# Optimization experiments

Measured on AMD Instinct MI355X. Metric: run time of the kernel, lower is better.

## Reference

```python
import jax, jax.numpy as jnp
import numpy as np

B, C_IN, T = 16, 1, 10240
C = 256                # conv_dim_out == config.model.conv_channels
KERNEL, STRIDE, PAD = 10, 5, 0
K_STEPS = 12           # config.model.predict_steps
NEG = 10               # config.train.neg_samples
EPS = 1e-5
L_OUT = (T + 2 * PAD - KERNEL) // STRIDE + 1   # 2047


def setup_inputs() -> dict:
    key = jax.random.key(0)
    ks = jax.random.split(key, 5)
    return {
        "x": jax.random.normal(ks[0], (B, C_IN, T), jnp.float32),
        "conv_w": jax.random.normal(ks[1], (C, C_IN, KERNEL), jnp.float32) * 0.1,
        "conv_b": jnp.zeros((C,), jnp.float32),
        "bn_gamma": jnp.ones((C,), jnp.float32),
        "bn_beta": jnp.zeros((C,), jnp.float32),
        "tr_w": jax.random.normal(ks[2], (K_STEPS, C, C), jnp.float32) / np.sqrt(C).astype(np.float32),
        "tr_b": jnp.zeros((K_STEPS, C), jnp.float32),
        "perm": jax.random.permutation(ks[3], L_OUT),  # randperm over the time axis
    }


def reference(x, conv_w, conv_b, bn_gamma, bn_beta, tr_w, tr_b, perm):
    # ---- encoder: Conv1d -> ReLU -> BatchNorm1d (training-mode batch stats) ----
    h = jax.lax.conv_general_dilated(
        x, conv_w, window_strides=(STRIDE,), padding=[(PAD, PAD)],
        dimension_numbers=("NCH", "OIH", "NCH"))
    h = jax.nn.relu(h + conv_b[None, :, None])            # (B, C, L)
    mu = h.mean(axis=(0, 2), keepdims=True)
    var = h.var(axis=(0, 2), keepdims=True)               # biased, as torch BN
    h = (h - mu) * jax.lax.rsqrt(var + EPS)
    h = h * bn_gamma[None, :, None] + bn_beta[None, :, None]
    z = h.transpose(0, 2, 1)                              # (B, L, C)

    # ---- negatives: batch-roll by 1, random permutation of the time axis; detached ----
    z_negative = jax.lax.stop_gradient(jnp.roll(z, 1, axis=0)[:, perm, :])

    L = z.shape[1]
    # z_neg_full[b, i] == roll(z_neg, i, axis=0)[b] == z_neg[(b - i) % B]
    roll_idx = (jnp.arange(B)[:, None] - jnp.arange(NEG)[None, :]) % B  # (B, NEG)

    losses = []
    for k in range(1, K_STEPS + 1):
        l_len = L - k
        z_pos = z[:, k:, :]                               # (B, l, C)
        z_neg = z_negative[:, k:, :]                      # (B, l, C)
        z_neg_full = z_neg[roll_idx]                      # (B, NEG, l, C)
        W, bb = tr_w[k - 1], tr_b[k - 1]
        est_pos = (z_pos @ W + bb)[:, None]               # (B, 1, l, C)
        est_neg = z_neg_full @ W + bb                     # (B, NEG, l, C)
        estimated = jnp.concatenate([est_pos, est_neg], axis=1)        # (B, S, l, C)
        z_full = jnp.concatenate([z_pos[:, None], z_neg_full], axis=1)  # (B, S, l, C)
        f = jnp.einsum("bslc,bslc->bsl", estimated, z_full)
        # faithful to torch: flatten (b, s, l) row-major then view as (b*l, S)
        f_k = f.reshape(B * l_len, NEG + 1)
        logp = jax.nn.log_softmax(f_k, axis=1)
        losses.append(-logp.sum() / ((l_len - k) * B))

    # torch forward returns z.permute(0, 2, 1); losses returned too for baseline use
    return z.transpose(0, 2, 1), jnp.stack(losses)
```

## Files before the change

kernel.cpp:

```cpp
#include <hip/hip_runtime.h>
#include <hip/hip_bf16.h>
#include <math.h>

constexpr int B_ = 16;
constexpr int T_ = 10240;
constexpr int C_ = 256;
constexpr int KW = 10;
constexpr int L_ = 2047;
constexpr int N_ = B_ * L_;
constexpr int KSTEPS = 12;
constexpr float EPS_ = 1e-5f;
constexpr int QSTR = 32768;

typedef short bf16x8 __attribute__((ext_vector_type(8)));
typedef float f32x4  __attribute__((ext_vector_type(4)));

__global__ __launch_bounds__(256) void stats_wt_kernel(
    const float* __restrict__ x, const float* __restrict__ cw, const float* __restrict__ cb,
    float* __restrict__ ssum, float* __restrict__ ssq,
    const float* __restrict__ tw, __hip_bfloat16* __restrict__ Wt)
{
    __shared__ float smem[64 * 65];
    const int bid = blockIdx.x;
    if (bid < 512) {
        const int b  = bid & 15;
        const int l0 = (bid >> 4) * 64;
        const int cnt = min(64, L_ - l0);
        const int c = threadIdx.x;
        float* xs = smem;
        const float* xb = x + (size_t)b * T_;
        for (int i = threadIdx.x; i < cnt * 5 + 5; i += 256) xs[i] = xb[l0 * 5 + i];
        float w[KW];
#pragma unroll
        for (int j = 0; j < KW; ++j) w[j] = cw[c * KW + j];
        const float bias = cb[c];
        __syncthreads();
        float s = 0.f, s2 = 0.f;
        float xw[KW];
#pragma unroll
        for (int j = 0; j < KW; ++j) xw[j] = xs[j];
#pragma unroll 2
        for (int dl = 0; dl < cnt; ++dl) {
            float v = bias;
#pragma unroll
            for (int j = 0; j < KW; ++j) v = fmaf(xw[j], w[j], v);
            v = fmaxf(v, 0.f);
            s += v;
            s2 = fmaf(v, v, s2);
#pragma unroll
            for (int j = 0; j < 5; ++j) xw[j] = xw[j + 5];
#pragma unroll
            for (int j = 0; j < 5; ++j) xw[j + 5] = xs[dl * 5 + 10 + j];
        }
        atomicAdd(&ssum[c], s);
        atomicAdd(&ssq[c], s2);
    } else {
        const int idx = bid - 512;
        const int k  = idx >> 4;
        const int c0 = ((idx & 15) >> 2) * 64, j0 = (idx & 3) * 64;
        float (*tile)[65] = (float(*)[65])smem;
        for (int i = threadIdx.x; i < 64 * 64; i += 256) {
            int c = i >> 6, j = i & 63;
            tile[c][j] = tw[((size_t)k * C_ + (c0 + c)) * C_ + j0 + j];
        }
        __syncthreads();
        for (int i = threadIdx.x; i < 64 * 64; i += 256) {
            int j = i >> 6, c = i & 63;
            Wt[((size_t)k * C_ + (j0 + j)) * C_ + c0 + c] = __float2bfloat16(tile[c][j]);
        }
    }
}

__global__ __launch_bounds__(256) void conv_norm_kernel(
    const float* __restrict__ x, const float* __restrict__ cw, const float* __restrict__ cb,
    const float* __restrict__ ssum, const float* __restrict__ ssq,
    const float* __restrict__ gamma, const float* __restrict__ beta,
    __hip_bfloat16* __restrict__ Zb, float* __restrict__ out0)
{
    const int b  = blockIdx.y;
    const int l0 = blockIdx.x * 32;
    const int cnt = min(32, L_ - l0);
    const int c = threadIdx.x;
    __shared__ float xs[32 * 5 + 8];
    __shared__ float zt[32][257];
    const float* xb = x + (size_t)b * T_;
    for (int i = threadIdx.x; i < cnt * 5 + 5; i += 256) xs[i] = xb[l0 * 5 + i];
    float w[KW];
#pragma unroll
    for (int j = 0; j < KW; ++j) w[j] = cw[c * KW + j];
    const float bias = cb[c];
    const float inv_n = 1.0f / (float)N_;
    const float mu  = ssum[c] * inv_n;
    const float var = ssq[c] * inv_n - mu * mu;
    const float sc  = gamma[c] * rsqrtf(var + EPS_);
    const float sh  = beta[c] - mu * sc;
    __syncthreads();
    for (int dl = 0; dl < cnt; ++dl) {
        float v = bias;
#pragma unroll
        for (int j = 0; j < KW; ++j) v = fmaf(xs[dl * 5 + j], w[j], v);
        v = fmaxf(v, 0.f);
        float z = fmaf(v, sc, sh);
        Zb[((size_t)(b * L_ + l0 + dl)) * C_ + c] = __float2bfloat16(z);
        zt[dl][c] = z;
    }
    __syncthreads();
    const int lq  = threadIdx.x & 31;
    const int cr0 = threadIdx.x >> 5;
    if (lq < cnt) {
#pragma unroll
        for (int i = 0; i < 32; ++i) {
            int cr = cr0 * 32 + i;
            out0[((size_t)(b * C_ + cr)) * L_ + l0 + lq] = zt[lq][cr];
        }
    }
}

__global__ __launch_bounds__(512, 4) void qmfma_kernel(
    const __hip_bfloat16* __restrict__ Zb, const __hip_bfloat16* __restrict__ Wt,
    const float* __restrict__ tb, float* __restrict__ qt)
{
    const int k   = blockIdx.y;
    const int grp = blockIdx.x;
    const __hip_bfloat16* __restrict__ Wk = Wt + (size_t)k * C_ * C_;

    __shared__ __hip_bfloat16 zs[4][32 * 256];
    __shared__ float qacc[8][256];

    const int tid  = threadIdx.x;
    const int lane = tid & 63, wave = tid >> 6;
    const int n16  = lane & 15, quad = lane >> 4;
    const int sw   = n16 & 7;
    const int row0 = grp * 8 * 32;

    bf16x8 wfrag[2][8];
    {
        const __hip_bfloat16* wb = Wk + ((size_t)(32 * wave + n16)) * C_ + quad * 8;
#pragma unroll
        for (int ct = 0; ct < 2; ++ct)
#pragma unroll
            for (int it = 0; it < 8; ++it)
                wfrag[ct][it] = *(const bf16x8*)(wb + ct * 16 * C_ + it * 32);
    }
    float4 bias4[2];
#pragma unroll
    for (int ct = 0; ct < 2; ++ct)
        bias4[ct] = *(const float4*)(tb + k * C_ + 32 * wave + ct * 16 + quad * 4);

#define STAGE(buf, t) do {                                                                  \
    _Pragma("unroll")                                                                       \
    for (int i_ = 0; i_ < 2; ++i_) {                                                        \
        int ch = i_ * 512 + wave * 64 + lane;                                               \
        int rr = ch >> 5;                                                                   \
        int rg = row0 + (t) * 32 + rr; if (rg > N_ - 1) rg = N_ - 1;                        \
        int jj = (lane & 31) ^ (rr & 7);                                                    \
        __builtin_amdgcn_global_load_lds(                                                   \
            (const __attribute__((address_space(1))) void*)(Zb + (size_t)rg * C_ + jj * 8), \
            (__attribute__((address_space(3))) void*)(&zs[buf][i_ * 4096 + wave * 512]),    \
            16, 0, 0);                                                                      \
    }                                                                                       \
} while (0)

    STAGE(0, 0);
    STAGE(1, 1);
    asm volatile("s_waitcnt vmcnt(0)" ::: "memory");

#pragma unroll
    for (int t = 0; t < 8; ++t) {
        if (t < 6) STAGE((t + 2) & 3, t + 2);
        if (t < 6)                { asm volatile("s_waitcnt vmcnt(4)" ::: "memory"); }
        else if (t == 6)          { asm volatile("s_waitcnt vmcnt(2)" ::: "memory"); }
        else                      { asm volatile("s_waitcnt vmcnt(0)" ::: "memory"); }
        __builtin_amdgcn_s_barrier();

        const __hip_bfloat16* zsp = (const __hip_bfloat16*)zs[t & 3];

        f32x4 acc[2][2];
#pragma unroll
        for (int rt = 0; rt < 2; ++rt)
#pragma unroll
            for (int ct = 0; ct < 2; ++ct) acc[rt][ct] = f32x4{0.f, 0.f, 0.f, 0.f};

        __builtin_amdgcn_s_setprio(1);
#pragma unroll
        for (int it = 0; it < 8; ++it) {
            const int js = (it * 4 + quad) ^ sw;
            bf16x8 zf0 = *(const bf16x8*)(zsp + n16 * 256 + js * 8);
            bf16x8 zf1 = *(const bf16x8*)(zsp + (n16 + 16) * 256 + js * 8);
#pragma unroll
            for (int ct = 0; ct < 2; ++ct) {
                acc[0][ct] = __builtin_amdgcn_mfma_f32_16x16x32_bf16(
                    wfrag[ct][it], zf0, acc[0][ct], 0, 0, 0);
                acc[1][ct] = __builtin_amdgcn_mfma_f32_16x16x32_bf16(
                    wfrag[ct][it], zf1, acc[1][ct], 0, 0, 0);
            }
        }
        __builtin_amdgcn_s_setprio(0);

#pragma unroll
        for (int rt = 0; rt < 2; ++rt) {
            const int row = rt * 16 + n16;
            float s = 0.f;
#pragma unroll
            for (int ct = 0; ct < 2; ++ct) {
                const int j  = 4 * wave + 2 * ct + (quad >> 1);
                const char* zp = (const char*)zsp + row * 512 + ((j ^ sw) << 4) + (quad & 1) * 8;
                uint2 zz = *(const uint2*)zp;
                float z0 = __uint_as_float(zz.x << 16);
                float z1 = __uint_as_float(zz.x & 0xffff0000u);
                float z2 = __uint_as_float(zz.y << 16);
                float z3 = __uint_as_float(zz.y & 0xffff0000u);
                s = fmaf(acc[rt][ct][0] + bias4[ct].x, z0, s);
                s = fmaf(acc[rt][ct][1] + bias4[ct].y, z1, s);
                s = fmaf(acc[rt][ct][2] + bias4[ct].z, z2, s);
                s = fmaf(acc[rt][ct][3] + bias4[ct].w, z3, s);
            }
            s += __shfl_xor(s, 16);
            s += __shfl_xor(s, 32);
            if (lane < 16) qacc[wave][t * 32 + row] = s;
        }
    }
#undef STAGE

    __syncthreads();
    if (tid < 256) {
        int rg = row0 + tid;
        if (rg < N_) {
            float qv = 0.f;
#pragma unroll
            for (int w2 = 0; w2 < 8; ++w2) qv += qacc[w2][tid];
            int b = rg / L_;
            int l = rg - b * L_;
            qt[(size_t)k * QSTR + (l << 4) + b] = qv;
        }
    }
}

__global__ __launch_bounds__(256) void loss_kernel(
    const float* __restrict__ qt, const int* __restrict__ perm, float* __restrict__ lpart)
{
    const int k = blockIdx.y + 1;
    const float* qk = qt + (size_t)(k - 1) * QSTR;
    const int nval = B_ * (L_ - k);
    const int idx = blockIdx.x * 256 + threadIdx.x;

    float contrib = 0.f;
    if (idx < nval) {
        int b = idx & 15;
        int l = k + (idx >> 4);
        float f0 = qk[(l << 4) | b];
        int pl = perm[l];
        const float* qn = qk + ((size_t)pl << 4);
        float f[10];
#pragma unroll
        for (int n = 0; n < 10; ++n) f[n] = qn[(b + 15 - n) & 15];
        float m = f0;
#pragma unroll
        for (int i = 0; i < 10; ++i) m = fmaxf(m, f[i]);
        float se = __expf(f0 - m), fs = f0;
#pragma unroll
        for (int i = 0; i < 10; ++i) { se += __expf(f[i] - m); fs += f[i]; }
        contrib = 11.f * (m + __logf(se)) - fs;
    }

    __shared__ float red[4];
#pragma unroll
    for (int off = 32; off > 0; off >>= 1) contrib += __shfl_down(contrib, off);
    const int lane = threadIdx.x & 63;
    const int wave = threadIdx.x >> 6;
    if (lane == 0) red[wave] = contrib;
    __syncthreads();
    if (threadIdx.x == 0)
        lpart[(size_t)(k - 1) * 128 + blockIdx.x] = red[0] + red[1] + red[2] + red[3];
}

__global__ __launch_bounds__(768) void finalize_loss_kernel(
    const float* __restrict__ lpart, float* __restrict__ out1)
{
    const int w = threadIdx.x >> 6;
    const int lane = threadIdx.x & 63;
    float v = lpart[(size_t)w * 128 + lane] + lpart[(size_t)w * 128 + lane + 64];
#pragma unroll
    for (int off = 32; off > 0; off >>= 1) v += __shfl_down(v, off);
    if (lane == 0) {
        float div = (float)((L_ - 2 * (w + 1)) * B_);
        out1[w] = v / div;
    }
}

extern "C" void kernel_launch(void* const* d_in, const int* in_sizes, int n_in,
                              void* d_out, int out_size, void* d_ws, size_t ws_size,
                              hipStream_t stream)
{
    const float* x     = (const float*)d_in[0];
    const float* cw    = (const float*)d_in[1];
    const float* cb    = (const float*)d_in[2];
    const float* gamma = (const float*)d_in[3];
    const float* beta  = (const float*)d_in[4];
    const float* tw    = (const float*)d_in[5];
    const float* tb    = (const float*)d_in[6];
    const int*   perm  = (const int*)d_in[7];

    float* out0 = (float*)d_out;
    float* out1 = out0 + (size_t)B_ * C_ * L_;

    char* ws = (char*)d_ws;
    __hip_bfloat16* Zb = (__hip_bfloat16*)ws;   ws += (size_t)N_ * C_ * 2;
    __hip_bfloat16* Wt = (__hip_bfloat16*)ws;   ws += (size_t)KSTEPS * C_ * C_ * 2;
    float* qt    = (float*)ws;                  ws += (size_t)KSTEPS * QSTR * 4;
    float* ssum  = (float*)ws;                  ws += C_ * 4;
    float* ssq   = (float*)ws;                  ws += C_ * 4;
    float* lpart = (float*)ws;                  ws += (size_t)KSTEPS * 128 * 4;

    hipMemsetAsync(ssum, 0, 2 * C_ * sizeof(float), stream);

    stats_wt_kernel<<<704, 256, 0, stream>>>(x, cw, cb, ssum, ssq, tw, Wt);

    dim3 gcv(64, 16);
    conv_norm_kernel<<<gcv, 256, 0, stream>>>(x, cw, cb, ssum, ssq, gamma, beta, Zb, out0);

    dim3 gq(128, KSTEPS);
    qmfma_kernel<<<gq, 512, 0, stream>>>(Zb, Wt, tb, qt);

    dim3 gl(128, KSTEPS);
    loss_kernel<<<gl, 256, 0, stream>>>(qt, perm, lpart);
    finalize_loss_kernel<<<1, 768, 0, stream>>>(lpart, out1);
}
```

Measured before the change: 172.9 us.

## Fuse conv stats and normalize into one cooperative kernel with grid syncs

Merges the stats/weight-transpose kernel and the conv/normalize kernel into a single cooperative launch over 1024 blocks. Grid-wide syncs handle zeroing the accumulators and the BN statistics reduction. Each block keeps its pre-norm conv outputs in shared memory so the convolution is not recomputed, and the partial sums are spread over 8 slots to reduce atomic contention. This drops the memset and one kernel launch, but it requires all 1024 blocks to be co-resident and adds two grid barriers.

```diff
diff --git a/kernel.cpp b/kernel.cpp
--- a/kernel.cpp
+++ b/kernel.cpp
@@ -1,6 +1,9 @@
 #include <hip/hip_runtime.h>
 #include <hip/hip_bf16.h>
+#include <hip/hip_cooperative_groups.h>
 #include <math.h>
+
+namespace cg = cooperative_groups;
 
 constexpr int B_ = 16;
 constexpr int T_ = 10240;
@@ -15,103 +18,94 @@
 typedef short bf16x8 __attribute__((ext_vector_type(8)));
 typedef float f32x4  __attribute__((ext_vector_type(4)));
 
-__global__ __launch_bounds__(256) void stats_wt_kernel(
+__global__ __launch_bounds__(256, 4) void convstats_kernel(
     const float* __restrict__ x, const float* __restrict__ cw, const float* __restrict__ cb,
-    float* __restrict__ ssum, float* __restrict__ ssq,
-    const float* __restrict__ tw, __hip_bfloat16* __restrict__ Wt)
-{
-    __shared__ float smem[64 * 65];
-    const int bid = blockIdx.x;
-    if (bid < 512) {
-        const int b  = bid & 15;
-        const int l0 = (bid >> 4) * 64;
-        const int cnt = min(64, L_ - l0);
-        const int c = threadIdx.x;
-        float* xs = smem;
-        const float* xb = x + (size_t)b * T_;
-        for (int i = threadIdx.x; i < cnt * 5 + 5; i += 256) xs[i] = xb[l0 * 5 + i];
-        float w[KW];
-#pragma unroll
-        for (int j = 0; j < KW; ++j) w[j] = cw[c * KW + j];
-        const float bias = cb[c];
-        __syncthreads();
-        float s = 0.f, s2 = 0.f;
-        float xw[KW];
-#pragma unroll
-        for (int j = 0; j < KW; ++j) xw[j] = xs[j];
-#pragma unroll 2
-        for (int dl = 0; dl < cnt; ++dl) {
-            float v = bias;
-#pragma unroll
-            for (int j = 0; j < KW; ++j) v = fmaf(xw[j], w[j], v);
-            v = fmaxf(v, 0.f);
-            s += v;
-            s2 = fmaf(v, v, s2);
-#pragma unroll
-            for (int j = 0; j < 5; ++j) xw[j] = xw[j + 5];
-#pragma unroll
-            for (int j = 0; j < 5; ++j) xw[j + 5] = xs[dl * 5 + 10 + j];
-        }
-        atomicAdd(&ssum[c], s);
-        atomicAdd(&ssq[c], s2);
-    } else {
-        const int idx = bid - 512;
-        const int k  = idx >> 4;
-        const int c0 = ((idx & 15) >> 2) * 64, j0 = (idx & 3) * 64;
-        float (*tile)[65] = (float(*)[65])smem;
-        for (int i = threadIdx.x; i < 64 * 64; i += 256) {
-            int c = i >> 6, j = i & 63;
-            tile[c][j] = tw[((size_t)k * C_ + (c0 + c)) * C_ + j0 + j];
-        }
-        __syncthreads();
-        for (int i = threadIdx.x; i < 64 * 64; i += 256) {
-            int j = i >> 6, c = i & 63;
-            Wt[((size_t)k * C_ + (j0 + j)) * C_ + c0 + c] = __float2bfloat16(tile[c][j]);
-        }
-    }
-}
-
-__global__ __launch_bounds__(256) void conv_norm_kernel(
-    const float* __restrict__ x, const float* __restrict__ cw, const float* __restrict__ cb,
-    const float* __restrict__ ssum, const float* __restrict__ ssq,
     const float* __restrict__ gamma, const float* __restrict__ beta,
+    const float* __restrict__ tw, __hip_bfloat16* __restrict__ Wt,
+    float* __restrict__ ssum8, float* __restrict__ ssq8,
     __hip_bfloat16* __restrict__ Zb, float* __restrict__ out0)
 {
+    __shared__ float xs[32 * 5 + 8];
+    __shared__ float zt[32][257];
+    __shared__ float scS[256], shS[256];
+
+    const int lt = blockIdx.x;
     const int b  = blockIdx.y;
-    const int l0 = blockIdx.x * 32;
+    const int flat = b * 64 + lt;
+    const int l0 = lt * 32;
     const int cnt = min(32, L_ - l0);
     const int c = threadIdx.x;
-    __shared__ float xs[32 * 5 + 8];
-    __shared__ float zt[32][257];
+
+    if (flat == 0) {
+        for (int i = c; i < 8 * 256; i += 256) { ssum8[i] = 0.f; ssq8[i] = 0.f; }
+    }
+
     const float* xb = x + (size_t)b * T_;
-    for (int i = threadIdx.x; i < cnt * 5 + 5; i += 256) xs[i] = xb[l0 * 5 + i];
+    for (int i = c; i < cnt * 5 + 5; i += 256) xs[i] = xb[l0 * 5 + i];
     float w[KW];
 #pragma unroll
     for (int j = 0; j < KW; ++j) w[j] = cw[c * KW + j];
     const float bias = cb[c];
+    __syncthreads();
+
+    cg::this_grid().sync();
+
+    float s = 0.f, s2 = 0.f;
+    for (int dl = 0; dl < cnt; ++dl) {
+        float v = bias;
+#pragma unroll
+        for (int j = 0; j < KW; ++j) v = fmaf(xs[dl * 5 + j], w[j], v);
+        v = fmaxf(v, 0.f);
+        zt[dl][c] = v;
+        s += v;
+        s2 = fmaf(v, v, s2);
+    }
+    atomicAdd(&ssum8[(lt & 7) * 256 + c], s);
+    atomicAdd(&ssq8[(lt & 7) * 256 + c], s2);
+
+    cg::this_grid().sync();
+
+    float su = 0.f, sq = 0.f;
+#pragma unroll
+    for (int i = 0; i < 8; ++i) { su += ssum8[i * 256 + c]; sq += ssq8[i * 256 + c]; }
     const float inv_n = 1.0f / (float)N_;
-    const float mu  = ssum[c] * inv_n;
-    const float var = ssq[c] * inv_n - mu * mu;
+    const float mu  = su * inv_n;
+    const float var = sq * inv_n - mu * mu;
     const float sc  = gamma[c] * rsqrtf(var + EPS_);
     const float sh  = beta[c] - mu * sc;
+    scS[c] = sc; shS[c] = sh;
     __syncthreads();
+
     for (int dl = 0; dl < cnt; ++dl) {
-        float v = bias;
-#pragma unroll
-        for (int j = 0; j < KW; ++j) v = fmaf(xs[dl * 5 + j], w[j], v);
-        v = fmaxf(v, 0.f);
-        float z = fmaf(v, sc, sh);
+        float z = fmaf(zt[dl][c], sc, sh);
         Zb[((size_t)(b * L_ + l0 + dl)) * C_ + c] = __float2bfloat16(z);
-        zt[dl][c] = z;
-    }
-    __syncthreads();
-    const int lq  = threadIdx.x & 31;
-    const int cr0 = threadIdx.x >> 5;
-    if (lq < cnt) {
-#pragma unroll
-        for (int i = 0; i < 32; ++i) {
-            int cr = cr0 * 32 + i;
-            out0[((size_t)(b * C_ + cr)) * L_ + l0 + lq] = zt[lq][cr];
+    }
+    {
+        const int lq  = threadIdx.x & 31;
+        const int cr0 = threadIdx.x >> 5;
+        if (lq < cnt) {
+#pragma unroll
+            for (int i = 0; i < 32; ++i) {
+                int cr = cr0 * 32 + i;
+                out0[((size_t)(b * C_ + cr)) * L_ + l0 + lq] =
+                    fmaf(zt[lq][cr], scS[cr], shS[cr]);
+            }
+        }
+    }
+
+    if (flat < 192) {
+        __syncthreads();
+        float (*tile)[65] = (float(*)[65])zt;
+        const int k  = flat >> 4;
+        const int c0 = ((flat & 15) >> 2) * 64, j0 = (flat & 3) * 64;
+        for (int i = c; i < 64 * 64; i += 256) {
+            int cc = i >> 6, j = i & 63;
+            tile[cc][j] = tw[((size_t)k * C_ + (c0 + cc)) * C_ + j0 + j];
+        }
+        __syncthreads();
+        for (int i = c; i < 64 * 64; i += 256) {
+            int j = i >> 6, cc = i & 63;
+            Wt[((size_t)k * C_ + (j0 + j)) * C_ + c0 + cc] = __float2bfloat16(tile[cc][j]);
         }
     }
 }
@@ -308,16 +302,15 @@
     __hip_bfloat16* Zb = (__hip_bfloat16*)ws;   ws += (size_t)N_ * C_ * 2;
     __hip_bfloat16* Wt = (__hip_bfloat16*)ws;   ws += (size_t)KSTEPS * C_ * C_ * 2;
     float* qt    = (float*)ws;                  ws += (size_t)KSTEPS * QSTR * 4;
-    float* ssum  = (float*)ws;                  ws += C_ * 4;
-    float* ssq   = (float*)ws;                  ws += C_ * 4;
+    float* ssum8 = (float*)ws;                  ws += 8 * C_ * 4;
+    float* ssq8  = (float*)ws;                  ws += 8 * C_ * 4;
     float* lpart = (float*)ws;                  ws += (size_t)KSTEPS * 128 * 4;
 
-    hipMemsetAsync(ssum, 0, 2 * C_ * sizeof(float), stream);
-
-    stats_wt_kernel<<<704, 256, 0, stream>>>(x, cw, cb, ssum, ssq, tw, Wt);
-
-    dim3 gcv(64, 16);
-    conv_norm_kernel<<<gcv, 256, 0, stream>>>(x, cw, cb, ssum, ssq, gamma, beta, Zb, out0);
+    void* cargs[] = { (void*)&x, (void*)&cw, (void*)&cb, (void*)&gamma, (void*)&beta,
+                      (void*)&tw, (void*)&Wt, (void*)&ssum8, (void*)&ssq8,
+                      (void*)&Zb, (void*)&out0 };
+    hipLaunchCooperativeKernel((const void*)convstats_kernel,
+                               dim3(64, 16), dim3(256), cargs, 0, stream);
 
     dim3 gq(128, KSTEPS);
     qmfma_kernel<<<gq, 512, 0, stream>>>(Zb, Wt, tb, qt);
```

Measured after the change: 322.4 us. +86.5%, slower.
